# Optimization experiments

Hardware: AMD Instinct MI355X
Metric: run time of the kernel (lower is better)

## Reference

```python
import jax, jax.numpy as jnp
import numpy as np

B, N, D = 1, 2048, 2048
H, DH, DR, MP = 16, 128, 64, 4
LOCAL = H * DH // MP  # per-shard qkv width
ATTN_MASK_VALUE = -1e10
LN_EPS = 1e-5


def setup_inputs() -> dict:
    key = jax.random.key(0)
    ks = jax.random.split(key, 5)
    s = 0.02
    return {
        "x": jax.random.normal(ks[0], (B, N, D), jnp.float32),
        "ln_scale": jnp.ones((D,), jnp.float32),
        "ln_offset": jnp.zeros((D,), jnp.float32),
        "w_qkv": jax.random.normal(ks[1], (D, 3 * H * DH), jnp.float32) * s,
        "w_attn_out": jax.random.normal(ks[2], (H * DH, D), jnp.float32) * s,
        "w_ff_in": jax.random.normal(ks[3], (D, 4 * D), jnp.float32) * s,
        "b_ff_in": jnp.zeros((4 * D,), jnp.float32),
        "w_ff_out": jax.random.normal(ks[4], (4 * D, D), jnp.float32) * s,
        "b_ff_out": jnp.zeros((D,), jnp.float32),
    }


def _rotate_every_two(x):
    # (..., d) -> interleaved (-x2, x1) pairs, GPT-J style
    x1 = x[..., ::2]
    x2 = x[..., 1::2]
    return jnp.stack((-x2, x1), axis=-1).reshape(x.shape)


def _fixed_pos_embedding(n, dim):
    inv_freq = 1.0 / (10000.0 ** (np.arange(0, dim, 2, dtype=np.float32) / dim))
    ang = np.einsum("i,j->ij", np.arange(n, dtype=np.float32), inv_freq)  # [n, dim/2]
    return jnp.asarray(np.sin(ang), jnp.float32), jnp.asarray(np.cos(ang), jnp.float32)


def _apply_rotary(x, sin, cos):
    # x: [b, n, h, d_rot]; sin/cos: [n, d_rot/2] repeated pairwise -> [1, n, 1, d_rot]
    sin = jnp.repeat(sin, 2, axis=-1)[None, :, None, :]
    cos = jnp.repeat(cos, 2, axis=-1)[None, :, None, :]
    return x * cos + _rotate_every_two(x) * sin


def reference(x, ln_scale, ln_offset, w_qkv, w_attn_out, w_ff_in, b_ff_in, w_ff_out, b_ff_out):
    # ---- LayerNorm (shared input to parallel attn + FFN) ----
    mu = jnp.mean(x, axis=-1, keepdims=True)
    var = jnp.var(x, axis=-1, keepdims=True)
    h = (x - mu) * jax.lax.rsqrt(var + LN_EPS) * ln_scale + ln_offset

    # ---- Causal self-attention with partial rotary ----
    qkv = (h @ w_qkv).reshape(B, N, MP, 3 * LOCAL)  # mp-sharded layout
    q, v, k = jnp.split(qkv, [LOCAL, 2 * LOCAL], axis=-1)
    heads = lambda t: t.reshape(B, N, H, DH)  # shard_heads: [b,n,mp,local] -> [b,n,h,dh]
    q, v, k = heads(q), heads(v), heads(k)

    sin, cos = _fixed_pos_embedding(N, DR)
    q = jnp.concatenate([_apply_rotary(q[..., :DR], sin, cos), q[..., DR:]], axis=-1)
    k = jnp.concatenate([_apply_rotary(k[..., :DR], sin, cos), k[..., DR:]], axis=-1)

    attn_scale = np.float32(np.sqrt(DH))
    logits = jnp.einsum("bihd,bjhd->bhij", q, k) / attn_scale
    causal_mask = jnp.triu(jnp.ones((N, N), dtype=bool), 1)
    logits = jnp.where(causal_mask, ATTN_MASK_VALUE, logits)
    attn_w = jax.nn.softmax(logits, axis=-1)
    attn_vec = jnp.einsum("bhij,bjhd->bihd", attn_w, v).reshape(B, N, H * DH)
    attn_out = attn_vec @ w_attn_out

    # ---- FFN (parallel branch, same LN input) ----
    ff_out = jax.nn.gelu(h @ w_ff_in + b_ff_in) @ w_ff_out + b_ff_out

    return attn_out + ff_out
```

## Files before the change

kernel.cpp:

```cpp
#include <hip/hip_runtime.h>
#include <hip/hip_bf16.h>

using bf16_t = __hip_bfloat16;
typedef __attribute__((ext_vector_type(8))) __bf16 bfrag;
typedef __attribute__((ext_vector_type(4))) float f32x4;

#define MFMA16(a, b, c) __builtin_amdgcn_mfma_f32_16x16x32_bf16((a), (b), (c), 0, 0, 0)

__device__ __forceinline__ void gload_lds16(const void* g, void* l) {
  __builtin_amdgcn_global_load_lds((const __attribute__((address_space(1))) void*)g,
                                   (__attribute__((address_space(3))) void*)l, 16, 0, 0);
}

__global__ __launch_bounds__(256) void transpose_cvt(const float* __restrict__ in,
    bf16_t* __restrict__ out, int K, int N) {
  __shared__ float t[32][33];
  const int n0 = blockIdx.x * 32, k0 = blockIdx.y * 32;
  const int tx = threadIdx.x & 31, ty = threadIdx.x >> 5;
#pragma unroll
  for (int i = 0; i < 4; ++i)
    t[ty + i * 8][tx] = in[(size_t)(k0 + ty + i * 8) * N + n0 + tx];
  __syncthreads();
#pragma unroll
  for (int i = 0; i < 4; ++i)
    out[(size_t)(n0 + ty + i * 8) * K + k0 + tx] = bf16_t(t[tx][ty + i * 8]);
}

__global__ __launch_bounds__(256) void ln_kernel(const float* __restrict__ x,
    const float* __restrict__ sc, const float* __restrict__ of, bf16_t* __restrict__ h) {
  __shared__ float red[8];
  const int n = blockIdx.x, tid = threadIdx.x;
  const float* xr = x + (size_t)n * 2048;
  float4 a = ((const float4*)xr)[tid * 2];
  float4 b = ((const float4*)xr)[tid * 2 + 1];
  float s = a.x + a.y + a.z + a.w + b.x + b.y + b.z + b.w;
  float q = a.x * a.x + a.y * a.y + a.z * a.z + a.w * a.w +
            b.x * b.x + b.y * b.y + b.z * b.z + b.w * b.w;
#pragma unroll
  for (int m = 32; m; m >>= 1) { s += __shfl_xor(s, m); q += __shfl_xor(q, m); }
  if ((tid & 63) == 0) { red[(tid >> 6) * 2] = s; red[(tid >> 6) * 2 + 1] = q; }
  __syncthreads();
  s = red[0] + red[2] + red[4] + red[6];
  q = red[1] + red[3] + red[5] + red[7];
  const float mu = s * (1.f / 2048.f);
  const float inv = rsqrtf(q * (1.f / 2048.f) - mu * mu + 1e-5f);
  const int base = tid * 8;
  float v[8] = {a.x, a.y, a.z, a.w, b.x, b.y, b.z, b.w};
  bf16_t* hr = h + (size_t)n * 2048 + base;
#pragma unroll
  for (int j = 0; j < 8; ++j) hr[j] = bf16_t((v[j] - mu) * inv * sc[base + j] + of[base + j]);
}

template <int EPI>
__global__ __launch_bounds__(512, 2) void gemm8p(
    const bf16_t* __restrict__ A, int lda, const bf16_t* __restrict__ BT, int ldb,
    const float* __restrict__ bias, float* __restrict__ Cf, bf16_t* __restrict__ Cb,
    int M, int N, int K, size_t splitStride) {
  extern __shared__ __align__(16) char lds[];
  const int tid = threadIdx.x, wid = tid >> 6, lane = tid & 63;
  const int lc = lane & 15, lg = lane >> 4;
  const int bm = blockIdx.y * 256, bn = blockIdx.x * 256;
  const int wr = wid >> 2, wc = wid & 3;
  const int NT = K >> 6;
  const bf16_t* Ab = A + (size_t)blockIdx.z * K;
  const bf16_t* Bb = BT + (size_t)blockIdx.z * K;
  const int sr = wid * 16 + (lane >> 2);
  const int lgp = (lane & 3) ^ ((sr >> 1) & 3);

  auto stageS = [&](int s) {
    if (s >= 4 * NT) return;
    const int ts = s >> 2, hs = s & 3, dd = ts & 1, kk = hs >> 1;
    const int koff = ts * 64 + kk * 32;
    const int slotOff = ((hs & 1) ? 65536 : 0) + ((dd * 2 + kk) << 14);
    const bf16_t* X = (hs & 1) ? Bb : Ab;
    const int R0 = (hs & 1) ? bn : bm;
    const int ld = (hs & 1) ? ldb : lda;
    char* base = lds + slotOff + wid * 1024;
    gload_lds16(X + (size_t)(R0 + sr) * ld + koff + lgp * 8, base);
    gload_lds16(X + (size_t)(R0 + 128 + sr) * ld + koff + lgp * 8, base + 8192);
  };

#pragma unroll
  for (int s = 0; s < 7; ++s) stageS(s);
  asm volatile("s_waitcnt vmcnt(6)" ::: "memory");
  __builtin_amdgcn_s_barrier();

  f32x4 acc[8][4] = {};
#define FR(off, row) \
  (*(const bfrag*)(lds + (off) + (row) * 64 + ((lg ^ (((row) >> 1) & 3)) << 4)))

  for (int t = 0; t < NT; ++t) {
    const int d = t & 1;
    const int aoff0 = (d * 2 + 0) << 14, aoff1 = (d * 2 + 1) << 14;
    const int boff0 = 65536 + aoff0, boff1 = 65536 + aoff1;
    bfrag a[8];
    {
#pragma unroll
      for (int m = 0; m < 8; ++m) a[m] = FR(aoff0, wr * 128 + m * 16 + lc);
      bfrag b0 = FR(boff0, wc * 64 + lc);
      bfrag b1 = FR(boff0, wc * 64 + 16 + lc);
      stageS(4 * t + 7);
      __builtin_amdgcn_s_barrier();
      asm volatile("s_waitcnt lgkmcnt(0)" ::: "memory");
      __builtin_amdgcn_sched_barrier(0);
      __builtin_amdgcn_s_setprio(1);
#pragma unroll
      for (int m = 0; m < 8; ++m) {
        acc[m][0] = MFMA16(a[m], b0, acc[m][0]);
        acc[m][1] = MFMA16(a[m], b1, acc[m][1]);
      }
      __builtin_amdgcn_s_setprio(0);
      __builtin_amdgcn_s_barrier();
    }
    {
      bfrag b2 = FR(boff0, wc * 64 + 32 + lc);
      bfrag b3 = FR(boff0, wc * 64 + 48 + lc);
      stageS(4 * t + 8);
      __builtin_amdgcn_s_barrier();
      asm volatile("s_waitcnt lgkmcnt(0)" ::: "memory");
      __builtin_amdgcn_sched_barrier(0);
      __builtin_amdgcn_s_setprio(1);
#pragma unroll
      for (int m = 0; m < 8; ++m) {
        acc[m][2] = MFMA16(a[m], b2, acc[m][2]);
        acc[m][3] = MFMA16(a[m], b3, acc[m][3]);
      }
      __builtin_amdgcn_s_setprio(0);
      __builtin_amdgcn_s_barrier();
    }
    {
#pragma unroll
      for (int m = 0; m < 8; ++m) a[m] = FR(aoff1, wr * 128 + m * 16 + lc);
      bfrag b0 = FR(boff1, wc * 64 + lc);
      bfrag b1 = FR(boff1, wc * 64 + 16 + lc);
      stageS(4 * t + 9);
      __builtin_amdgcn_s_barrier();
      asm volatile("s_waitcnt lgkmcnt(0)" ::: "memory");
      __builtin_amdgcn_sched_barrier(0);
      __builtin_amdgcn_s_setprio(1);
#pragma unroll
      for (int m = 0; m < 8; ++m) {
        acc[m][0] = MFMA16(a[m], b0, acc[m][0]);
        acc[m][1] = MFMA16(a[m], b1, acc[m][1]);
      }
      __builtin_amdgcn_s_setprio(0);
      __builtin_amdgcn_s_barrier();
    }
    {
      bfrag b2 = FR(boff1, wc * 64 + 32 + lc);
      bfrag b3 = FR(boff1, wc * 64 + 48 + lc);
      stageS(4 * t + 10);
      __builtin_amdgcn_s_barrier();
      asm volatile("s_waitcnt lgkmcnt(0)" ::: "memory");
      __builtin_amdgcn_sched_barrier(0);
      __builtin_amdgcn_s_setprio(1);
#pragma unroll
      for (int m = 0; m < 8; ++m) {
        acc[m][2] = MFMA16(a[m], b2, acc[m][2]);
        acc[m][3] = MFMA16(a[m], b3, acc[m][3]);
      }
      __builtin_amdgcn_s_setprio(0);
      if (t < NT - 2) asm volatile("s_waitcnt vmcnt(6)" ::: "memory");
      else            asm volatile("s_waitcnt vmcnt(0)" ::: "memory");
      __builtin_amdgcn_s_barrier();
    }
  }
#undef FR
  float* Cfz = Cf + (size_t)blockIdx.z * splitStride;
  const int row0 = bm + wr * 128 + lg * 4;
  const int col0 = bn + wc * 64 + lc;
#pragma unroll
  for (int m = 0; m < 8; ++m) {
#pragma unroll
    for (int n = 0; n < 4; ++n) {
      const int col = col0 + n * 16;
      float bv = (EPI & 1) ? bias[col] : 0.f;
#pragma unroll
      for (int i = 0; i < 4; ++i) {
        const int row = row0 + m * 16 + i;
        float v = acc[m][n][i];
        if (EPI & 1) v += bv;
        if (EPI & 2) v = 0.5f * v * (1.f + tanhf(0.7978845608028654f * (v + 0.044715f * v * v * v)));
        if (EPI & 8) Cb[(size_t)row * N + col] = bf16_t(v);
        else         Cfz[(size_t)row * N + col] = v;
      }
    }
  }
}

template <int NP, bool ADDIN, bool BIAS>
__global__ __launch_bounds__(256) void reduceP(const float* __restrict__ p0,
    const float* __restrict__ p1, const float* __restrict__ p2,
    const float* __restrict__ p3, const float* __restrict__ bias,
    float* __restrict__ out, int total, int colmask) {
  const int i = (blockIdx.x * 256 + threadIdx.x) * 4;
  if (i >= total) return;
  float4 v = *(const float4*)(p0 + i);
  float4 w = *(const float4*)(p1 + i);
  v.x += w.x; v.y += w.y; v.z += w.z; v.w += w.w;
  if (NP == 4) {
    float4 u = *(const float4*)(p2 + i);
    float4 z = *(const float4*)(p3 + i);
    v.x += u.x + z.x; v.y += u.y + z.y; v.z += u.z + z.z; v.w += u.w + z.w;
  }
  if (BIAS) {
    float4 b = *(const float4*)(bias + (i & colmask));
    v.x += b.x; v.y += b.y; v.z += b.z; v.w += b.w;
  }
  if (ADDIN) {
    float4 o = *(const float4*)(out + i);
    v.x += o.x; v.y += o.y; v.z += o.z; v.w += o.w;
  }
  *(float4*)(out + i) = v;
}

__global__ __launch_bounds__(128) void rope_kernel(const bf16_t* __restrict__ qkv,
    bf16_t* __restrict__ qh, bf16_t* __restrict__ kh, bf16_t* __restrict__ vT) {
  const int n = blockIdx.x, hh = blockIdx.y;
  const int d = threadIdx.x;
  const int mp = hh >> 2, hi = hh & 3;
  const bf16_t* row = qkv + (size_t)n * 6144 + mp * 1536 + hi * 128;
  float q = __bfloat162float(row[d]);
  float k = __bfloat162float(row[1024 + d]);
  if (d < 64) {
    const float ang = (float)n * powf(10000.f, -(float)(d & ~1) / 64.f);
    const float sn = sinf(ang), cs = cosf(ang);
    const float qp = __shfl_xor(q, 1), kp = __shfl_xor(k, 1);
    if (d & 1) { q = q * cs + qp * sn; k = k * cs + kp * sn; }
    else       { q = q * cs - qp * sn; k = k * cs - kp * sn; }
  }
  qh[((size_t)hh * 2048 + n) * 128 + d] = bf16_t(q * 0.08838834764831845f);
  kh[((size_t)hh * 2048 + n) * 128 + d] = bf16_t(k);
  vT[((size_t)hh * 128 + d) * 2048 + n] = row[512 + d];
}

__global__ __launch_bounds__(256) void attn_kernel(const bf16_t* __restrict__ qh,
    const bf16_t* __restrict__ kh, const bf16_t* __restrict__ vT, bf16_t* __restrict__ av) {
  __shared__ alignas(16) char Kbuf[2][16384];
  __shared__ alignas(16) char Vbuf[2][16384];
  __shared__ alignas(16) bf16_t Ps[4][16 * 72];
  const int p = blockIdx.x, h = blockIdx.y;
  const int tid = threadIdx.x, wid = tid >> 6, lane = tid & 63;
  const int lc = lane & 15, lg = lane >> 4;
  const int krow = wid * 4 + (lane >> 4);
  const int vrow = wid * 8 + (lane >> 3);

  auto stage = [&](int kv0, int d) {
#pragma unroll
    for (int i = 0; i < 4; ++i) {
      const int kr = i * 16 + krow;
      const int kch = (lane & 15) ^ (kr & 15);
      gload_lds16(kh + ((size_t)h * 2048 + kv0 + kr) * 128 + kch * 8,
                  Kbuf[d] + i * 4096 + wid * 1024);
      const int vr = i * 32 + vrow;
      const int vch = (lane & 7) ^ (vr & 7);
      gload_lds16(vT + ((size_t)h * 128 + vr) * 2048 + kv0 + vch * 8,
                  Vbuf[d] + i * 4096 + wid * 1024);
    }
  };
#define FRK(d, row, ch) (*(const bfrag*)(Kbuf[d] + (row) * 256 + (((ch) ^ ((row) & 15)) << 4)))
#define FRV(d, row, ch) (*(const bfrag*)(Vbuf[d] + (row) * 128 + (((ch) ^ ((row) & 7)) << 4)))

#pragma unroll 1
  for (int half = 0; half < 2; ++half) {
    const int qt = half ? (31 - p) : p;
    const int nkv = qt + 1;
    const int qr = qt * 64 + wid * 16;
    const bf16_t* Qb = qh + ((size_t)h * 2048 + qr) * 128;
    bfrag qf[4];
#pragma unroll
    for (int ks = 0; ks < 4; ++ks)
      qf[ks] = *(const bfrag*)&Qb[lc * 128 + ks * 32 + lg * 8];
    f32x4 O[8] = {};
    float mr[4] = {-1e30f, -1e30f, -1e30f, -1e30f};
    float lsum[4] = {0.f, 0.f, 0.f, 0.f};

    stage(0, 0);
    asm volatile("s_waitcnt vmcnt(0)" ::: "memory");
    __builtin_amdgcn_s_barrier();

#pragma unroll 1
    for (int kt = 0; kt < nkv; ++kt) {
      const int d = kt & 1;
      const int kv0 = kt * 64;
      if (kt + 1 < nkv) stage(kv0 + 64, d ^ 1);
      f32x4 s[4];
#pragma unroll
      for (int c = 0; c < 4; ++c) {
        f32x4 a = {};
#pragma unroll
        for (int ks = 0; ks < 4; ++ks) {
          bfrag kf = FRK(d, c * 16 + lc, ks * 4 + lg);
          a = MFMA16(qf[ks], kf, a);
        }
        s[c] = a;
      }
      if (kt == qt) {
#pragma unroll
        for (int c = 0; c < 4; ++c)
#pragma unroll
          for (int i = 0; i < 4; ++i)
            if (kv0 + c * 16 + lc > qr + lg * 4 + i) s[c][i] = -1e10f;
      }
      float pm[4];
#pragma unroll
      for (int i = 0; i < 4; ++i)
        pm[i] = fmaxf(fmaxf(s[0][i], s[1][i]), fmaxf(s[2][i], s[3][i]));
#pragma unroll
      for (int m = 1; m < 16; m <<= 1)
#pragma unroll
        for (int i = 0; i < 4; ++i) pm[i] = fmaxf(pm[i], __shfl_xor(pm[i], m));
      float al[4], rs[4];
#pragma unroll
      for (int i = 0; i < 4; ++i) {
        const float mn = fmaxf(mr[i], pm[i]);
        al[i] = __expf(mr[i] - mn);
        mr[i] = mn;
        rs[i] = 0.f;
      }
#pragma unroll
      for (int c = 0; c < 4; ++c)
#pragma unroll
        for (int i = 0; i < 4; ++i) {
          const float pv = __expf(s[c][i] - mr[i]);
          s[c][i] = pv; rs[i] += pv;
        }
#pragma unroll
      for (int m = 1; m < 16; m <<= 1)
#pragma unroll
        for (int i = 0; i < 4; ++i) rs[i] += __shfl_xor(rs[i], m);
#pragma unroll
      for (int i = 0; i < 4; ++i) lsum[i] = lsum[i] * al[i] + rs[i];
#pragma unroll
      for (int n = 0; n < 8; ++n)
#pragma unroll
        for (int i = 0; i < 4; ++i) O[n][i] *= al[i];
#pragma unroll
      for (int c = 0; c < 4; ++c)
#pragma unroll
        for (int i = 0; i < 4; ++i)
          Ps[wid][(lg * 4 + i) * 72 + c * 16 + lc] = bf16_t(s[c][i]);
#pragma unroll
      for (int k2 = 0; k2 < 2; ++k2) {
        bfrag pf = *(const bfrag*)((const char*)&Ps[wid][0] + lc * 144 + k2 * 64 + lg * 16);
#pragma unroll
        for (int n = 0; n < 8; ++n) {
          bfrag vf = FRV(d, n * 16 + lc, k2 * 4 + lg);
          O[n] = MFMA16(pf, vf, O[n]);
        }
      }
      if (kt + 1 < nkv) asm volatile("s_waitcnt vmcnt(0)" ::: "memory");
      asm volatile("s_waitcnt lgkmcnt(0)" ::: "memory");
      __builtin_amdgcn_s_barrier();
    }
#pragma unroll
    for (int n = 0; n < 8; ++n)
#pragma unroll
      for (int i = 0; i < 4; ++i)
        av[(size_t)(qr + lg * 4 + i) * 2048 + h * 128 + n * 16 + lc] = bf16_t(O[n][i] / lsum[i]);
    __builtin_amdgcn_s_barrier();
  }
#undef FRK
#undef FRV
}

extern "C" void kernel_launch(void* const* d_in, const int* in_sizes, int n_in,
                              void* d_out, int out_size, void* d_ws, size_t ws_size,
                              hipStream_t stream) {
  const float* x        = (const float*)d_in[0];
  const float* ln_scale = (const float*)d_in[1];
  const float* ln_offset= (const float*)d_in[2];
  const float* w_qkv    = (const float*)d_in[3];
  const float* w_ao     = (const float*)d_in[4];
  const float* w_ff_in  = (const float*)d_in[5];
  const float* b_ff_in  = (const float*)d_in[6];
  const float* w_ff_out = (const float*)d_in[7];
  const float* b_ff_out = (const float*)d_in[8];
  float* out = (float*)d_out;

  char* ws = (char*)d_ws;
  bf16_t* wqkvT   = (bf16_t*)(ws);
  bf16_t* waoT    = (bf16_t*)(ws + 25165824);
  bf16_t* wffinT  = (bf16_t*)(ws + 33554432);
  bf16_t* wffoutT = (bf16_t*)(ws + 67108864);
  bf16_t* h       = (bf16_t*)(ws + 100663296);
  bf16_t* qhb     = (bf16_t*)(ws + 109051904);
  bf16_t* khb     = (bf16_t*)(ws + 117440512);
  bf16_t* vTb     = (bf16_t*)(ws + 125829120);
  bf16_t* avb     = (bf16_t*)(ws + 134217728);
  bf16_t* qkvb    = (bf16_t*)(ws + 142606336);
  bf16_t* ff1b    = qkvb;
  float*  pa      = (float*)(ws + 142606336);
  float*  pf      = (float*)(ws);

  hipFuncSetAttribute((const void*)gemm8p<0>,  hipFuncAttributeMaxDynamicSharedMemorySize, 131072);
  hipFuncSetAttribute((const void*)gemm8p<8>,  hipFuncAttributeMaxDynamicSharedMemorySize, 131072);
  hipFuncSetAttribute((const void*)gemm8p<11>, hipFuncAttributeMaxDynamicSharedMemorySize, 131072);

  dim3 b256(256), b512(512);
  transpose_cvt<<<dim3(192, 64),  b256, 0, stream>>>(w_qkv,    wqkvT,   2048, 6144);
  transpose_cvt<<<dim3(64, 64),   b256, 0, stream>>>(w_ao,     waoT,    2048, 2048);
  transpose_cvt<<<dim3(256, 64),  b256, 0, stream>>>(w_ff_in,  wffinT,  2048, 8192);
  transpose_cvt<<<dim3(64, 256),  b256, 0, stream>>>(w_ff_out, wffoutT, 8192, 2048);
  ln_kernel<<<dim3(2048), b256, 0, stream>>>(x, ln_scale, ln_offset, h);

  gemm8p<8><<<dim3(24, 8, 1), b512, 131072, stream>>>(h, 2048, wqkvT, 2048,
      nullptr, nullptr, qkvb, 2048, 6144, 2048, 0);
  rope_kernel<<<dim3(2048, 16), dim3(128), 0, stream>>>(qkvb, qhb, khb, vTb);
  attn_kernel<<<dim3(16, 16), b256, 0, stream>>>(qhb, khb, vTb, avb);

  gemm8p<0><<<dim3(8, 8, 2), b512, 131072, stream>>>(avb, 2048, waoT, 2048,
      nullptr, pa, nullptr, 2048, 2048, 1024, (size_t)2048 * 2048);
  reduceP<2, false, false><<<dim3(4096), b256, 0, stream>>>(pa, pa + 4194304,
      nullptr, nullptr, nullptr, out, 4194304, 2047);

  gemm8p<11><<<dim3(32, 8, 1), b512, 131072, stream>>>(h, 2048, wffinT, 2048,
      b_ff_in, nullptr, ff1b, 2048, 8192, 2048, 0);

  gemm8p<0><<<dim3(8, 8, 4), b512, 131072, stream>>>(ff1b, 8192, wffoutT, 8192,
      nullptr, pf, nullptr, 2048, 2048, 2048, (size_t)2048 * 2048);
  reduceP<4, true, true><<<dim3(4096), b256, 0, stream>>>(pf, pf + 4194304,
      pf + 2 * 4194304, pf + 3 * 4194304, b_ff_out, out, 4194304, 2047);
}
```

Before: 446.8 us.

## Restructure GEMM main loop with register-prefetched fragments and XCD-aware block swizzle

Reworks the 256x256 GEMM inner loop so each phase computes a 4x4 block of MFMAs from fragments already loaded by the previous phase. The LDS reads for the next phase are issued before the barrier, with partial lgkmcnt waits instead of full drains. Global-to-LDS staging switches to pointer-increment lambdas with a reordered prefetch schedule and an adjusted vmcnt depth. Workgroup IDs are also remapped round-robin across 8 groups to improve L2 locality per XCD. This adds register pressure and fragile waitcnt accounting in exchange for better overlap of LDS reads with MFMA.

```diff
diff --git a/kernel.cpp b/kernel.cpp
--- a/kernel.cpp
+++ b/kernel.cpp
@@ -59,108 +59,121 @@
   extern __shared__ __align__(16) char lds[];
   const int tid = threadIdx.x, wid = tid >> 6, lane = tid & 63;
   const int lc = lane & 15, lg = lane >> 4;
-  const int bm = blockIdx.y * 256, bn = blockIdx.x * 256;
+  const int nwg = gridDim.x * gridDim.y;
+  const int orig = blockIdx.y * gridDim.x + blockIdx.x;
+  const int wg = (orig & 7) * (nwg >> 3) + (orig >> 3);
+  const int bm = (wg / gridDim.x) * 256, bn = (wg % gridDim.x) * 256;
   const int wr = wid >> 2, wc = wid & 3;
   const int NT = K >> 6;
-  const bf16_t* Ab = A + (size_t)blockIdx.z * K;
-  const bf16_t* Bb = BT + (size_t)blockIdx.z * K;
   const int sr = wid * 16 + (lane >> 2);
   const int lgp = (lane & 3) ^ ((sr >> 1) & 3);
-
-  auto stageS = [&](int s) {
-    if (s >= 4 * NT) return;
-    const int ts = s >> 2, hs = s & 3, dd = ts & 1, kk = hs >> 1;
-    const int koff = ts * 64 + kk * 32;
-    const int slotOff = ((hs & 1) ? 65536 : 0) + ((dd * 2 + kk) << 14);
-    const bf16_t* X = (hs & 1) ? Bb : Ab;
-    const int R0 = (hs & 1) ? bn : bm;
-    const int ld = (hs & 1) ? ldb : lda;
-    char* base = lds + slotOff + wid * 1024;
-    gload_lds16(X + (size_t)(R0 + sr) * ld + koff + lgp * 8, base);
-    gload_lds16(X + (size_t)(R0 + 128 + sr) * ld + koff + lgp * 8, base + 8192);
-  };
-
-#pragma unroll
-  for (int s = 0; s < 7; ++s) stageS(s);
-  asm volatile("s_waitcnt vmcnt(6)" ::: "memory");
+  const size_t rA = (size_t)128 * lda, rB = (size_t)128 * ldb;
+  const bf16_t* pA0 = A + (size_t)blockIdx.z * K + (size_t)(bm + sr) * lda + lgp * 8;
+  const bf16_t* pA1 = pA0 + 32;
+  const bf16_t* pB0 = BT + (size_t)blockIdx.z * K + (size_t)(bn + sr) * ldb + lgp * 8;
+  const bf16_t* pB1 = pB0 + 32;
+  auto stA0 = [&](int ts) { char* b = lds + (((ts & 1) * 2 + 0) << 14) + wid * 1024;
+    gload_lds16(pA0, b); gload_lds16(pA0 + rA, b + 8192); pA0 += 64; };
+  auto stA1 = [&](int ts) { char* b = lds + (((ts & 1) * 2 + 1) << 14) + wid * 1024;
+    gload_lds16(pA1, b); gload_lds16(pA1 + rA, b + 8192); pA1 += 64; };
+  auto stB0 = [&](int ts) { char* b = lds + 65536 + (((ts & 1) * 2 + 0) << 14) + wid * 1024;
+    gload_lds16(pB0, b); gload_lds16(pB0 + rB, b + 8192); pB0 += 64; };
+  auto stB1 = [&](int ts) { char* b = lds + 65536 + (((ts & 1) * 2 + 1) << 14) + wid * 1024;
+    gload_lds16(pB1, b); gload_lds16(pB1 + rB, b + 8192); pB1 += 64; };
+
+  stA0(0); stB0(0); stA1(0); stB1(0); stA0(1); stB0(1); stA1(1);
+  asm volatile("s_waitcnt vmcnt(10)" ::: "memory");
   __builtin_amdgcn_s_barrier();
 
-  f32x4 acc[8][4] = {};
 #define FR(off, row) \
   (*(const bfrag*)(lds + (off) + (row) * 64 + ((lg ^ (((row) >> 1) & 3)) << 4)))
 
+  f32x4 acc[8][4] = {};
+  bfrag a0[4], a1v[4], a2v[4], a3v[4], bA[4], bB[4];
+#pragma unroll
+  for (int m = 0; m < 4; ++m) a0[m] = FR(0, wr * 128 + m * 16 + lc);
+#pragma unroll
+  for (int n = 0; n < 4; ++n) bA[n] = FR(65536, wc * 64 + n * 16 + lc);
+
+#pragma unroll 2
   for (int t = 0; t < NT; ++t) {
     const int d = t & 1;
     const int aoff0 = (d * 2 + 0) << 14, aoff1 = (d * 2 + 1) << 14;
     const int boff0 = 65536 + aoff0, boff1 = 65536 + aoff1;
-    bfrag a[8];
+    const int an0 = ((d ^ 1) * 2) << 14, bn0 = 65536 + an0;
     {
 #pragma unroll
-      for (int m = 0; m < 8; ++m) a[m] = FR(aoff0, wr * 128 + m * 16 + lc);
-      bfrag b0 = FR(boff0, wc * 64 + lc);
-      bfrag b1 = FR(boff0, wc * 64 + 16 + lc);
-      stageS(4 * t + 7);
-      __builtin_amdgcn_s_barrier();
-      asm volatile("s_waitcnt lgkmcnt(0)" ::: "memory");
+      for (int m = 0; m < 4; ++m) a1v[m] = FR(aoff0, wr * 128 + (4 + m) * 16 + lc);
+      asm volatile("s_waitcnt lgkmcnt(4)" ::: "memory");
       __builtin_amdgcn_sched_barrier(0);
+      __builtin_amdgcn_s_barrier();
+      if (t + 1 < NT) stB1(t + 1);
       __builtin_amdgcn_s_setprio(1);
 #pragma unroll
-      for (int m = 0; m < 8; ++m) {
-        acc[m][0] = MFMA16(a[m], b0, acc[m][0]);
-        acc[m][1] = MFMA16(a[m], b1, acc[m][1]);
-      }
+      for (int m = 0; m < 4; ++m)
+#pragma unroll
+        for (int n = 0; n < 4; ++n) acc[m][n] = MFMA16(a0[m], bA[n], acc[m][n]);
       __builtin_amdgcn_s_setprio(0);
+      if (t < NT - 2) asm volatile("s_waitcnt vmcnt(8)" ::: "memory");
+      else            asm volatile("s_waitcnt vmcnt(0)" ::: "memory");
       __builtin_amdgcn_s_barrier();
     }
     {
-      bfrag b2 = FR(boff0, wc * 64 + 32 + lc);
-      bfrag b3 = FR(boff0, wc * 64 + 48 + lc);
-      stageS(4 * t + 8);
-      __builtin_amdgcn_s_barrier();
-      asm volatile("s_waitcnt lgkmcnt(0)" ::: "memory");
+#pragma unroll
+      for (int m = 0; m < 4; ++m) a2v[m] = FR(aoff1, wr * 128 + m * 16 + lc);
+#pragma unroll
+      for (int n = 0; n < 4; ++n) bB[n] = FR(boff1, wc * 64 + n * 16 + lc);
+      asm volatile("s_waitcnt lgkmcnt(8)" ::: "memory");
       __builtin_amdgcn_sched_barrier(0);
+      __builtin_amdgcn_s_barrier();
+      if (t + 2 < NT) stA0(t + 2);
       __builtin_amdgcn_s_setprio(1);
 #pragma unroll
-      for (int m = 0; m < 8; ++m) {
-        acc[m][2] = MFMA16(a[m], b2, acc[m][2]);
-        acc[m][3] = MFMA16(a[m], b3, acc[m][3]);
-      }
+      for (int m = 0; m < 4; ++m)
+#pragma unroll
+        for (int n = 0; n < 4; ++n) acc[4 + m][n] = MFMA16(a1v[m], bA[n], acc[4 + m][n]);
       __builtin_amdgcn_s_setprio(0);
+      if (t < NT - 2) asm volatile("s_waitcnt vmcnt(8)" ::: "memory");
+      else            asm volatile("s_waitcnt vmcnt(0)" ::: "memory");
       __builtin_amdgcn_s_barrier();
     }
     {
 #pragma unroll
-      for (int m = 0; m < 8; ++m) a[m] = FR(aoff1, wr * 128 + m * 16 + lc);
-      bfrag b0 = FR(boff1, wc * 64 + lc);
-      bfrag b1 = FR(boff1, wc * 64 + 16 + lc);
-      stageS(4 * t + 9);
-      __builtin_amdgcn_s_barrier();
-      asm volatile("s_waitcnt lgkmcnt(0)" ::: "memory");
+      for (int m = 0; m < 4; ++m) a3v[m] = FR(aoff1, wr * 128 + (4 + m) * 16 + lc);
+      asm volatile("s_waitcnt lgkmcnt(4)" ::: "memory");
       __builtin_amdgcn_sched_barrier(0);
+      __builtin_amdgcn_s_barrier();
+      if (t + 2 < NT) stB0(t + 2);
       __builtin_amdgcn_s_setprio(1);
 #pragma unroll
-      for (int m = 0; m < 8; ++m) {
-        acc[m][0] = MFMA16(a[m], b0, acc[m][0]);
-        acc[m][1] = MFMA16(a[m], b1, acc[m][1]);
-      }
+      for (int m = 0; m < 4; ++m)
+#pragma unroll
+        for (int n = 0; n < 4; ++n) acc[m][n] = MFMA16(a2v[m], bB[n], acc[m][n]);
       __builtin_amdgcn_s_setprio(0);
+      if (t < NT - 2) asm volatile("s_waitcnt vmcnt(8)" ::: "memory");
+      else            asm volatile("s_waitcnt vmcnt(0)" ::: "memory");
       __builtin_amdgcn_s_barrier();
     }
     {
-      bfrag b2 = FR(boff1, wc * 64 + 32 + lc);
-      bfrag b3 = FR(boff1, wc * 64 + 48 + lc);
-      stageS(4 * t + 10);
-      __builtin_amdgcn_s_barrier();
-      asm volatile("s_waitcnt lgkmcnt(0)" ::: "memory");
+      if (t + 1 < NT) {
+#pragma unroll
+        for (int m = 0; m < 4; ++m) a0[m] = FR(an0, wr * 128 + m * 16 + lc);
+#pragma unroll
+        for (int n = 0; n < 4; ++n) bA[n] = FR(bn0, wc * 64 + n * 16 + lc);
+        asm volatile("s_waitcnt lgkmcnt(8)" ::: "memory");
+      } else {
+        asm volatile("s_waitcnt lgkmcnt(0)" ::: "memory");
+      }
       __builtin_amdgcn_sched_barrier(0);
+      __builtin_amdgcn_s_barrier();
+      if (t + 2 < NT) stA1(t + 2);
       __builtin_amdgcn_s_setprio(1);
 #pragma unroll
-      for (int m = 0; m < 8; ++m) {
-        acc[m][2] = MFMA16(a[m], b2, acc[m][2]);
-        acc[m][3] = MFMA16(a[m], b3, acc[m][3]);
-      }
+      for (int m = 0; m < 4; ++m)
+#pragma unroll
+        for (int n = 0; n < 4; ++n) acc[4 + m][n] = MFMA16(a3v[m], bB[n], acc[4 + m][n]);
       __builtin_amdgcn_s_setprio(0);
-      if (t < NT - 2) asm volatile("s_waitcnt vmcnt(6)" ::: "memory");
+      if (t < NT - 2) asm volatile("s_waitcnt vmcnt(8)" ::: "memory");
       else            asm volatile("s_waitcnt vmcnt(0)" ::: "memory");
       __builtin_amdgcn_s_barrier();
     }
```

Result: no change. 455.6 us (+2.0%).

## Stage GEMM epilogue through LDS for vectorized stores and simplify prefetch addressing

Applied to the files above, without the earlier changes.

The GEMM epilogue now writes accumulator tiles into a per-wave LDS scratch region, padded to a 72-element row stride, then reads them back as 16-byte vectors. This produces coalesced uint4/float4 global stores instead of scattered scalar bf16/float stores. The generic stageS lambda is replaced by four specialized staging lambdas with incrementing pointers, which removes per-call index arithmetic and branching. The extra LDS round trip adds latency and reuses the LDS buffers after the main loop.

```diff
diff --git a/kernel.cpp b/kernel.cpp
--- a/kernel.cpp
+++ b/kernel.cpp
@@ -62,26 +62,23 @@
   const int bm = blockIdx.y * 256, bn = blockIdx.x * 256;
   const int wr = wid >> 2, wc = wid & 3;
   const int NT = K >> 6;
-  const bf16_t* Ab = A + (size_t)blockIdx.z * K;
-  const bf16_t* Bb = BT + (size_t)blockIdx.z * K;
   const int sr = wid * 16 + (lane >> 2);
   const int lgp = (lane & 3) ^ ((sr >> 1) & 3);
-
-  auto stageS = [&](int s) {
-    if (s >= 4 * NT) return;
-    const int ts = s >> 2, hs = s & 3, dd = ts & 1, kk = hs >> 1;
-    const int koff = ts * 64 + kk * 32;
-    const int slotOff = ((hs & 1) ? 65536 : 0) + ((dd * 2 + kk) << 14);
-    const bf16_t* X = (hs & 1) ? Bb : Ab;
-    const int R0 = (hs & 1) ? bn : bm;
-    const int ld = (hs & 1) ? ldb : lda;
-    char* base = lds + slotOff + wid * 1024;
-    gload_lds16(X + (size_t)(R0 + sr) * ld + koff + lgp * 8, base);
-    gload_lds16(X + (size_t)(R0 + 128 + sr) * ld + koff + lgp * 8, base + 8192);
-  };
-
-#pragma unroll
-  for (int s = 0; s < 7; ++s) stageS(s);
+  const size_t rA = (size_t)128 * lda, rB = (size_t)128 * ldb;
+  const bf16_t* pA0 = A + (size_t)blockIdx.z * K + (size_t)(bm + sr) * lda + lgp * 8;
+  const bf16_t* pA1 = pA0 + 32;
+  const bf16_t* pB0 = BT + (size_t)blockIdx.z * K + (size_t)(bn + sr) * ldb + lgp * 8;
+  const bf16_t* pB1 = pB0 + 32;
+  auto stA0 = [&](int ts) { char* b = lds + (((ts & 1) * 2 + 0) << 14) + wid * 1024;
+    gload_lds16(pA0, b); gload_lds16(pA0 + rA, b + 8192); pA0 += 64; };
+  auto stA1 = [&](int ts) { char* b = lds + (((ts & 1) * 2 + 1) << 14) + wid * 1024;
+    gload_lds16(pA1, b); gload_lds16(pA1 + rA, b + 8192); pA1 += 64; };
+  auto stB0 = [&](int ts) { char* b = lds + 65536 + (((ts & 1) * 2 + 0) << 14) + wid * 1024;
+    gload_lds16(pB0, b); gload_lds16(pB0 + rB, b + 8192); pB0 += 64; };
+  auto stB1 = [&](int ts) { char* b = lds + 65536 + (((ts & 1) * 2 + 1) << 14) + wid * 1024;
+    gload_lds16(pB1, b); gload_lds16(pB1 + rB, b + 8192); pB1 += 64; };
+
+  stA0(0); stB0(0); stA1(0); stB1(0); stA0(1); stB0(1); stA1(1);
   asm volatile("s_waitcnt vmcnt(6)" ::: "memory");
   __builtin_amdgcn_s_barrier();
 
@@ -99,7 +96,7 @@
       for (int m = 0; m < 8; ++m) a[m] = FR(aoff0, wr * 128 + m * 16 + lc);
       bfrag b0 = FR(boff0, wc * 64 + lc);
       bfrag b1 = FR(boff0, wc * 64 + 16 + lc);
-      stageS(4 * t + 7);
+      if (t + 1 < NT) stB1(t + 1);
       __builtin_amdgcn_s_barrier();
       asm volatile("s_waitcnt lgkmcnt(0)" ::: "memory");
       __builtin_amdgcn_sched_barrier(0);
@@ -115,7 +112,7 @@
     {
       bfrag b2 = FR(boff0, wc * 64 + 32 + lc);
       bfrag b3 = FR(boff0, wc * 64 + 48 + lc);
-      stageS(4 * t + 8);
+      if (t + 2 < NT) stA0(t + 2);
       __builtin_amdgcn_s_barrier();
       asm volatile("s_waitcnt lgkmcnt(0)" ::: "memory");
       __builtin_amdgcn_sched_barrier(0);
@@ -133,7 +130,7 @@
       for (int m = 0; m < 8; ++m) a[m] = FR(aoff1, wr * 128 + m * 16 + lc);
       bfrag b0 = FR(boff1, wc * 64 + lc);
       bfrag b1 = FR(boff1, wc * 64 + 16 + lc);
-      stageS(4 * t + 9);
+      if (t + 2 < NT) stB0(t + 2);
       __builtin_amdgcn_s_barrier();
       asm volatile("s_waitcnt lgkmcnt(0)" ::: "memory");
       __builtin_amdgcn_sched_barrier(0);
@@ -149,7 +146,7 @@
     {
       bfrag b2 = FR(boff1, wc * 64 + 32 + lc);
       bfrag b3 = FR(boff1, wc * 64 + 48 + lc);
-      stageS(4 * t + 10);
+      if (t + 2 < NT) stA1(t + 2);
       __builtin_amdgcn_s_barrier();
       asm volatile("s_waitcnt lgkmcnt(0)" ::: "memory");
       __builtin_amdgcn_sched_barrier(0);
@@ -166,24 +163,71 @@
     }
   }
 #undef FR
-  float* Cfz = Cf + (size_t)blockIdx.z * splitStride;
-  const int row0 = bm + wr * 128 + lg * 4;
-  const int col0 = bn + wc * 64 + lc;
-#pragma unroll
-  for (int m = 0; m < 8; ++m) {
-#pragma unroll
-    for (int n = 0; n < 4; ++n) {
-      const int col = col0 + n * 16;
-      float bv = (EPI & 1) ? bias[col] : 0.f;
-#pragma unroll
-      for (int i = 0; i < 4; ++i) {
-        const int row = row0 + m * 16 + i;
-        float v = acc[m][n][i];
-        if (EPI & 1) v += bv;
-        if (EPI & 2) v = 0.5f * v * (1.f + tanhf(0.7978845608028654f * (v + 0.044715f * v * v * v)));
-        if (EPI & 8) Cb[(size_t)row * N + col] = bf16_t(v);
-        else         Cfz[(size_t)row * N + col] = v;
-      }
+  char* W = lds + wid * 16384;
+  if (EPI & 8) {
+    bf16_t* Wb = (bf16_t*)W;
+#pragma unroll
+    for (int mc = 0; mc < 2; ++mc) {
+#pragma unroll
+      for (int m4 = 0; m4 < 4; ++m4) {
+#pragma unroll
+        for (int n = 0; n < 4; ++n) {
+          const int col = bn + wc * 64 + n * 16 + lc;
+          float bv = (EPI & 1) ? bias[col] : 0.f;
+#pragma unroll
+          for (int i = 0; i < 4; ++i) {
+            float v = acc[mc * 4 + m4][n][i];
+            if (EPI & 1) v += bv;
+            if (EPI & 2) v = 0.5f * v * (1.f + tanhf(0.7978845608028654f * (v + 0.044715f * v * v * v)));
+            Wb[(m4 * 16 + lg * 4 + i) * 72 + n * 16 + lc] = bf16_t(v);
+          }
+        }
+      }
+      asm volatile("s_waitcnt lgkmcnt(0)" ::: "memory");
+      __builtin_amdgcn_sched_barrier(0);
+#pragma unroll
+      for (int p = 0; p < 8; ++p) {
+        const int rl = p * 8 + (lane >> 3), j = lane & 7;
+        uint4 v = *(const uint4*)&Wb[rl * 72 + j * 8];
+        const int grow = bm + wr * 128 + mc * 64 + rl;
+        const int gcol = bn + wc * 64 + j * 8;
+        *(uint4*)&Cb[(size_t)grow * N + gcol] = v;
+      }
+      asm volatile("s_waitcnt lgkmcnt(0)" ::: "memory");
+      __builtin_amdgcn_sched_barrier(0);
+    }
+  } else {
+    float* Wf = (float*)W;
+    float* Cfz = Cf + (size_t)blockIdx.z * splitStride;
+#pragma unroll
+    for (int mc = 0; mc < 4; ++mc) {
+#pragma unroll
+      for (int m2 = 0; m2 < 2; ++m2) {
+#pragma unroll
+        for (int n = 0; n < 4; ++n) {
+          const int col = bn + wc * 64 + n * 16 + lc;
+          float bv = (EPI & 1) ? bias[col] : 0.f;
+#pragma unroll
+          for (int i = 0; i < 4; ++i) {
+            float v = acc[mc * 2 + m2][n][i];
+            if (EPI & 1) v += bv;
+            if (EPI & 2) v = 0.5f * v * (1.f + tanhf(0.7978845608028654f * (v + 0.044715f * v * v * v)));
+            Wf[(m2 * 16 + lg * 4 + i) * 72 + n * 16 + lc] = v;
+          }
+        }
+      }
+      asm volatile("s_waitcnt lgkmcnt(0)" ::: "memory");
+      __builtin_amdgcn_sched_barrier(0);
+#pragma unroll
+      for (int p = 0; p < 8; ++p) {
+        const int rl = p * 4 + (lane >> 4), j = lane & 15;
+        float4 v = *(const float4*)&Wf[rl * 72 + j * 4];
+        const int grow = bm + wr * 128 + mc * 32 + rl;
+        const int gcol = bn + wc * 64 + j * 4;
+        *(float4*)&Cfz[(size_t)grow * N + gcol] = v;
+      }
+      asm volatile("s_waitcnt lgkmcnt(0)" ::: "memory");
+      __builtin_amdgcn_sched_barrier(0);
     }
   }
 }
```

New measurement: 452.2 us. No clear change (+1.2%).
